# Kernel tuning notes

Measured on AMD Instinct MI355X. Metric: run time of the kernel, lower is better.

The kernel has to match this reference:

```python
import jax, jax.numpy as jnp
import numpy as np

NUM_HEADS = 16


def setup_inputs() -> dict:
    key = jax.random.key(0)
    ks = jax.random.split(key, 6)
    B, S, D = 2, 2048, 1024
    hidden_states = jax.random.normal(ks[0], (B, S, D), dtype=jnp.float32)
    attention_mask = jnp.zeros((B, 1, 1, S), dtype=jnp.float32)  # additive mask
    # Linear weights stored as [in, out] (equivalent to torch weight.T)
    W_qkv = jax.random.normal(ks[1], (D, 3 * D), dtype=jnp.float32) * (1.0 / np.sqrt(D))
    b_qkv = jnp.zeros((3 * D,), dtype=jnp.float32)
    W_proj = jax.random.normal(ks[2], (D, D), dtype=jnp.float32) * (1.0 / np.sqrt(D))
    b_proj = jnp.zeros((D,), dtype=jnp.float32)
    return {
        "hidden_states": hidden_states,
        "attention_mask": attention_mask,
        "W_qkv": W_qkv,
        "b_qkv": b_qkv,
        "W_proj": W_proj,
        "b_proj": b_proj,
    }


def reference(hidden_states, attention_mask, W_qkv, b_qkv, W_proj, b_proj):
    B, S, D = hidden_states.shape
    H = NUM_HEADS
    hd = D // H
    scale = 1.0 / jnp.sqrt(jnp.asarray(hd, hidden_states.dtype))

    qkv = hidden_states @ W_qkv + b_qkv            # [B,S,3D]
    q, k, v = jnp.split(qkv, 3, axis=-1)
    # [B,S,D] -> [B,H,S,hd]
    split_heads = lambda t: t.reshape(B, S, H, hd).transpose(0, 2, 1, 3)
    q, k, v = split_heads(q), split_heads(k), split_heads(v)

    scores = jnp.einsum("bhqd,bhkd->bhqk", q, k) * scale + attention_mask
    attn = jax.nn.softmax(scores, axis=-1)
    ctx = jnp.einsum("bhqk,bhkd->bhqd", attn, v)   # [B,H,S,hd]
    ctx = ctx.transpose(0, 2, 1, 3).reshape(B, S, D)
    return ctx @ W_proj + b_proj
```

## Files before the change

kernel.cpp:

```cpp
#include <hip/hip_runtime.h>
#include <hip/hip_bf16.h>

typedef short short8 __attribute__((ext_vector_type(8)));
typedef float floatx4 __attribute__((ext_vector_type(4)));
typedef int intx4 __attribute__((ext_vector_type(4)));

#define S_LEN 2048
#define DMODEL 1024
#define NH 16
#define HD 64
#define BATCH 2

static __device__ __forceinline__ short f2bf(float x) {
    __hip_bfloat16 h = __float2bfloat16(x);
    return *(short*)&h;
}

static __device__ __forceinline__ unsigned pk2(float lo, float hi) {
    unsigned a = (unsigned)(unsigned short)f2bf(lo);
    unsigned b = (unsigned)(unsigned short)f2bf(hi);
    return a | (b << 16);
}

static __device__ __forceinline__ void async_ld16(const __hip_bfloat16* g, __hip_bfloat16* l) {
    __builtin_amdgcn_global_load_lds(
        (const __attribute__((address_space(1))) unsigned int*)g,
        (__attribute__((address_space(3))) unsigned int*)l, 16, 0, 0);
}

__global__ __launch_bounds__(256) void cvt_kernel(const float* __restrict__ X,
                                                  __hip_bfloat16* __restrict__ Y) {
    int i = (blockIdx.x * 256 + threadIdx.x) * 8;
    floatx4 f0 = *(const floatx4*)&X[i];
    floatx4 f1 = *(const floatx4*)&X[i + 4];
    short8 s;
    s[0] = f2bf(f0[0]); s[1] = f2bf(f0[1]); s[2] = f2bf(f0[2]); s[3] = f2bf(f0[3]);
    s[4] = f2bf(f1[0]); s[5] = f2bf(f1[1]); s[6] = f2bf(f1[2]); s[7] = f2bf(f1[3]);
    *(short8*)&Y[i] = s;
}

__global__ void transpose_kernel(const float* __restrict__ W,
                                 __hip_bfloat16* __restrict__ Wt, int K, int N) {
    __shared__ float tile[32][33];
    int n0 = blockIdx.x * 32, k0 = blockIdx.y * 32;
    int tx = threadIdx.x, ty = threadIdx.y;
#pragma unroll
    for (int i = 0; i < 32; i += 8)
        tile[ty + i][tx] = W[(size_t)(k0 + ty + i) * N + n0 + tx];
    __syncthreads();
#pragma unroll
    for (int i = 0; i < 32; i += 8)
        Wt[(size_t)(n0 + ty + i) * K + k0 + tx] = __float2bfloat16(tile[tx][ty + i]);
}

__global__ __launch_bounds__(256) void gemm128(
    const __hip_bfloat16* __restrict__ A, const __hip_bfloat16* __restrict__ Bt,
    const float* __restrict__ bias, float* __restrict__ Cf,
    __hip_bfloat16* __restrict__ Qp, __hip_bfloat16* __restrict__ Kp,
    __hip_bfloat16* __restrict__ Vt, int M, int N, int K, int mode) {
    __shared__ __align__(16) __hip_bfloat16 As[128 * 32];
    __shared__ __align__(16) __hip_bfloat16 Bs[128 * 32];
    const int m0 = blockIdx.y * 128, n0 = blockIdx.x * 128;
    const int t = threadIdx.x;
    const int wave = t >> 6, lane = t & 63;
    const int quad = lane >> 4, m16 = lane & 15;
    const int wm = (wave >> 1) * 64, wn = (wave & 1) * 64;
    const int srow = lane >> 2, scol = (lane & 3) * 8;

    floatx4 acc[4][4] = {};
    for (int k0 = 0; k0 < K; k0 += 32) {
#pragma unroll
        for (int i = 0; i < 2; i++) {
            const int rbase = wave * 32 + i * 16;
            async_ld16(&A[(size_t)(m0 + rbase + srow) * K + k0 + scol], &As[rbase * 32]);
            async_ld16(&Bt[(size_t)(n0 + rbase + srow) * K + k0 + scol], &Bs[rbase * 32]);
        }
        __syncthreads();
        short8 af[4], bfr[4];
#pragma unroll
        for (int i = 0; i < 4; i++)
            af[i] = *(const short8*)&As[(wm + i * 16 + m16) * 32 + quad * 8];
#pragma unroll
        for (int j = 0; j < 4; j++)
            bfr[j] = *(const short8*)&Bs[(wn + j * 16 + m16) * 32 + quad * 8];
#pragma unroll
        for (int i = 0; i < 4; i++)
#pragma unroll
            for (int j = 0; j < 4; j++)
                acc[i][j] = __builtin_amdgcn_mfma_f32_16x16x32_bf16(af[i], bfr[j], acc[i][j], 0, 0, 0);
        __syncthreads();
    }
#pragma unroll
    for (int i = 0; i < 4; i++)
#pragma unroll
        for (int j = 0; j < 4; j++) {
            int col = n0 + wn + j * 16 + m16;
            float bv = bias[col];
#pragma unroll
            for (int r = 0; r < 4; r++) {
                int row = m0 + wm + i * 16 + quad * 4 + r;
                float v = acc[i][j][r] + bv;
                if (mode == 0) {
                    Cf[(size_t)row * N + col] = v;
                } else {
                    __hip_bfloat16 hv = __float2bfloat16(v);
                    int tt = col >> 10, rem = col & 1023;
                    int h = rem >> 6, d = rem & 63;
                    int b = row >> 11, s = row & 2047;
                    if (tt == 0)      Qp[((size_t)(b * NH + h) * S_LEN + s) * HD + d] = hv;
                    else if (tt == 1) Kp[((size_t)(b * NH + h) * S_LEN + s) * HD + d] = hv;
                    else              Vt[((size_t)(b * NH + h) * HD + d) * S_LEN + s] = hv;
                }
            }
        }
}

__global__ __launch_bounds__(256, 4) void attn_kernel(
    const __hip_bfloat16* __restrict__ Q,
    const __hip_bfloat16* __restrict__ K,
    const __hip_bfloat16* __restrict__ Vt,
    const float* __restrict__ mask,
    __hip_bfloat16* __restrict__ ctx) {
    __shared__ __align__(16) __hip_bfloat16 Ks[2][64 * 64];
    __shared__ __align__(16) __hip_bfloat16 Vs[2][64 * 64];
    const int bh = blockIdx.x;
    const int b = bh >> 4, h = bh & 15;
    const int t = threadIdx.x, wave = t >> 6, lane = t & 63;
    const int quad = lane >> 4, m16 = lane & 15;
    const int qbase = blockIdx.y * 64 + wave * 16;
    const __hip_bfloat16* Qh = Q + (size_t)bh * S_LEN * HD;
    const __hip_bfloat16* Kh = K + (size_t)bh * S_LEN * HD;
    const __hip_bfloat16* Vh = Vt + (size_t)bh * HD * S_LEN;
    const float* mb = mask + (size_t)b * S_LEN;
    const float LOG2E = 1.44269504f;
    const float scale2 = 0.125f * LOG2E;
    const float M_FIX2 = 20.0f * LOG2E;

    const int r8 = lane >> 3, c8 = lane & 7;
    const int kg0 = (wave * 16 + r8) * HD + ((c8 ^ r8) * 8);
    const int kg1 = (wave * 16 + 8 + r8) * HD + ((c8 ^ r8) * 8);
    const int vg0 = (wave * 16 + r8) * S_LEN + ((c8 ^ r8) * 8);
    const int vg1 = (wave * 16 + 8 + r8) * S_LEN + ((c8 ^ r8) * 8);

    short8 aq0 = *(const short8*)&Qh[(size_t)(qbase + m16) * HD + quad * 8];
    short8 aq1 = *(const short8*)&Qh[(size_t)(qbase + m16) * HD + 32 + quad * 8];

    const short ONEB = (short)0x3F80;
    const short8 ones = {ONEB, ONEB, ONEB, ONEB, ONEB, ONEB, ONEB, ONEB};

    {
        __hip_bfloat16* kd = &Ks[0][wave * 16 * 64];
        async_ld16(&Kh[kg0], kd);
        async_ld16(&Kh[kg1], kd + 512);
        __hip_bfloat16* vd = &Vs[0][wave * 16 * 64];
        async_ld16(&Vh[vg0], vd);
        async_ld16(&Vh[vg1], vd + 512);
    }
    __syncthreads();

    floatx4 o[4] = {};
    floatx4 lacc = {};
    const int swk = m16 & 7;
    const int e = quad & 1;
    const int cA = ((quad & 1) << 2) | (quad >> 1);
    const int cB = cA | 2;
    const int vsA = (cA ^ swk) * 8;
    const int vsB = (cB ^ swk) * 8;

    for (int it = 0; it < S_LEN / 64; it++) {
        const int k0 = it * 64;
        const int cur = it & 1;
        if (it < S_LEN / 64 - 1) {
            __hip_bfloat16* kd = &Ks[cur ^ 1][wave * 16 * 64];
            async_ld16(&Kh[(k0 + 64) * HD + kg0], kd);
            async_ld16(&Kh[(k0 + 64) * HD + kg1], kd + 512);
            __hip_bfloat16* vd = &Vs[cur ^ 1][wave * 16 * 64];
            async_ld16(&Vh[(k0 + 64) + vg0], vd);
            async_ld16(&Vh[(k0 + 64) + vg1], vd + 512);
        }

        const __hip_bfloat16* Kc = Ks[cur];
        floatx4 sc[4] = {};
        __builtin_amdgcn_s_setprio(1);
#pragma unroll
        for (int kt = 0; kt < 4; kt++) {
            const int row = kt * 16 + m16;
            short8 ak0 = *(const short8*)&Kc[row * 64 + ((quad ^ swk) * 8)];
            short8 ak1 = *(const short8*)&Kc[row * 64 + (((quad + 4) ^ swk) * 8)];
            sc[kt] = __builtin_amdgcn_mfma_f32_16x16x32_bf16(ak0, aq0, sc[kt], 0, 0, 0);
            sc[kt] = __builtin_amdgcn_mfma_f32_16x16x32_bf16(ak1, aq1, sc[kt], 0, 0, 0);
        }
        __builtin_amdgcn_s_setprio(0);

        unsigned dk[4][2];
#pragma unroll
        for (int kt = 0; kt < 4; kt++) {
            floatx4 mv = *(const floatx4*)&mb[k0 + kt * 16 + quad * 4];
            float p0 = __builtin_amdgcn_exp2f(
                __builtin_fmaf(sc[kt][0], scale2, __builtin_fmaf(mv[0], LOG2E, -M_FIX2)));
            float p1 = __builtin_amdgcn_exp2f(
                __builtin_fmaf(sc[kt][1], scale2, __builtin_fmaf(mv[1], LOG2E, -M_FIX2)));
            float p2 = __builtin_amdgcn_exp2f(
                __builtin_fmaf(sc[kt][2], scale2, __builtin_fmaf(mv[2], LOG2E, -M_FIX2)));
            float p3 = __builtin_amdgcn_exp2f(
                __builtin_fmaf(sc[kt][3], scale2, __builtin_fmaf(mv[3], LOG2E, -M_FIX2)));
            dk[kt][0] = pk2(p0, p1);
            dk[kt][1] = pk2(p2, p3);
        }

        unsigned t0 = e ? dk[0][0] : dk[2][0];
        unsigned t1 = e ? dk[0][1] : dk[2][1];
        unsigned t2 = e ? dk[1][0] : dk[3][0];
        unsigned t3 = e ? dk[1][1] : dk[3][1];
        unsigned r0 = (unsigned)__builtin_amdgcn_ds_swizzle((int)t0, 0x401F);
        unsigned r1 = (unsigned)__builtin_amdgcn_ds_swizzle((int)t1, 0x401F);
        unsigned r2 = (unsigned)__builtin_amdgcn_ds_swizzle((int)t2, 0x401F);
        unsigned r3 = (unsigned)__builtin_amdgcn_ds_swizzle((int)t3, 0x401F);
        intx4 wa, wb;
        wa[0] = (int)(e ? r0 : dk[0][0]);
        wa[1] = (int)(e ? r1 : dk[0][1]);
        wa[2] = (int)(e ? dk[2][0] : r0);
        wa[3] = (int)(e ? dk[2][1] : r1);
        wb[0] = (int)(e ? r2 : dk[1][0]);
        wb[1] = (int)(e ? r3 : dk[1][1]);
        wb[2] = (int)(e ? dk[3][0] : r2);
        wb[3] = (int)(e ? dk[3][1] : r3);
        short8 apA = *(short8*)&wa;
        short8 apB = *(short8*)&wb;

        const __hip_bfloat16* Vc = Vs[cur];
        __builtin_amdgcn_s_setprio(1);
        lacc = __builtin_amdgcn_mfma_f32_16x16x32_bf16(apA, ones, lacc, 0, 0, 0);
        lacc = __builtin_amdgcn_mfma_f32_16x16x32_bf16(apB, ones, lacc, 0, 0, 0);
#pragma unroll
        for (int tt = 0; tt < 4; tt++) {
            const int d = tt * 16 + m16;
            short8 bvA = *(const short8*)&Vc[d * 64 + vsA];
            short8 bvB = *(const short8*)&Vc[d * 64 + vsB];
            o[tt] = __builtin_amdgcn_mfma_f32_16x16x32_bf16(apA, bvA, o[tt], 0, 0, 0);
            o[tt] = __builtin_amdgcn_mfma_f32_16x16x32_bf16(apB, bvB, o[tt], 0, 0, 0);
        }
        __builtin_amdgcn_s_setprio(0);
        __syncthreads();
    }

    float li[4];
#pragma unroll
    for (int r = 0; r < 4; r++) li[r] = 1.0f / lacc[r];
#pragma unroll
    for (int tt = 0; tt < 4; tt++)
#pragma unroll
        for (int r = 0; r < 4; r++) {
            int srow = qbase + quad * 4 + r;
            int d = tt * 16 + m16;
            float v = o[tt][r] * li[r];
            ctx[((size_t)b * S_LEN + srow) * DMODEL + h * HD + d] = __float2bfloat16(v);
        }
}

extern "C" void kernel_launch(void* const* d_in, const int* in_sizes, int n_in,
                              void* d_out, int out_size, void* d_ws, size_t ws_size,
                              hipStream_t stream) {
    (void)in_sizes; (void)n_in; (void)out_size; (void)ws_size;
    const float* hidden = (const float*)d_in[0];
    const float* mask   = (const float*)d_in[1];
    const float* Wqkv   = (const float*)d_in[2];
    const float* bqkv   = (const float*)d_in[3];
    const float* Wproj  = (const float*)d_in[4];
    const float* bproj  = (const float*)d_in[5];
    float* out = (float*)d_out;

    __hip_bfloat16* ws = (__hip_bfloat16*)d_ws;
    const size_t Q4 = 4u * 1024 * 1024;
    __hip_bfloat16* Qp      = ws;
    __hip_bfloat16* Kp      = ws + 1 * Q4;
    __hip_bfloat16* Vt      = ws + 2 * Q4;
    __hip_bfloat16* hid_bf  = ws + 3 * Q4;
    __hip_bfloat16* ctx     = ws + 3 * Q4;
    __hip_bfloat16* Wqkv_t  = ws + 4 * Q4;
    __hip_bfloat16* Wproj_t = ws + 4 * Q4;

    cvt_kernel<<<dim3(4 * 1024 * 1024 / 2048), 256, 0, stream>>>(hidden, hid_bf);
    transpose_kernel<<<dim3(3072 / 32, 1024 / 32), dim3(32, 8), 0, stream>>>(Wqkv, Wqkv_t, 1024, 3072);

    gemm128<<<dim3(3072 / 128, 4096 / 128), 256, 0, stream>>>(
        hid_bf, Wqkv_t, bqkv, nullptr, Qp, Kp, Vt, BATCH * S_LEN, 3 * DMODEL, DMODEL, 1);

    transpose_kernel<<<dim3(1024 / 32, 1024 / 32), dim3(32, 8), 0, stream>>>(Wproj, Wproj_t, 1024, 1024);

    attn_kernel<<<dim3(BATCH * NH, S_LEN / 64), 256, 0, stream>>>(Qp, Kp, Vt, mask, ctx);

    gemm128<<<dim3(1024 / 128, 4096 / 128), 256, 0, stream>>>(
        ctx, Wproj_t, bproj, out, nullptr, nullptr, nullptr, BATCH * S_LEN, DMODEL, DMODEL, 0);
}
```

Baseline: 219.4 us.

## Split attention KV range across two wave teams and merge partials via LDS

The attention block grows from 256 to 512 threads: two teams of four waves each process half of the key sequence for the same 64 queries, using 32-key tiles with their own double-buffered LDS regions. At the end, team 1 writes its partial output and row sums to shared memory and team 0 adds them, normalizes, and writes ctx. The aim is more waves per CU and more latency hiding in the attention stage. The cost is smaller tiles with more barriers per key, an extra LDS exchange and barrier, and tighter register limits from launch_bounds(512,8).

```diff
diff --git a/kernel.cpp b/kernel.cpp
--- a/kernel.cpp
+++ b/kernel.cpp
@@ -115,19 +115,20 @@
         }
 }
 
-__global__ __launch_bounds__(256, 4) void attn_kernel(
+__global__ __launch_bounds__(512, 8) void attn_kernel(
     const __hip_bfloat16* __restrict__ Q,
     const __hip_bfloat16* __restrict__ K,
     const __hip_bfloat16* __restrict__ Vt,
     const float* __restrict__ mask,
     __hip_bfloat16* __restrict__ ctx) {
-    __shared__ __align__(16) __hip_bfloat16 Ks[2][64 * 64];
-    __shared__ __align__(16) __hip_bfloat16 Vs[2][64 * 64];
+    __shared__ __align__(16) __hip_bfloat16 smem[16384];
     const int bh = blockIdx.x;
     const int b = bh >> 4, h = bh & 15;
     const int t = threadIdx.x, wave = t >> 6, lane = t & 63;
+    const int team = wave >> 2, tw = wave & 3;
     const int quad = lane >> 4, m16 = lane & 15;
-    const int qbase = blockIdx.y * 64 + wave * 16;
+    const int qbase = blockIdx.y * 64 + tw * 16;
+    const int ko = team * (S_LEN / 2);
     const __hip_bfloat16* Qh = Q + (size_t)bh * S_LEN * HD;
     const __hip_bfloat16* Kh = K + (size_t)bh * S_LEN * HD;
     const __hip_bfloat16* Vh = Vt + (size_t)bh * HD * S_LEN;
@@ -136,11 +137,18 @@
     const float scale2 = 0.125f * LOG2E;
     const float M_FIX2 = 20.0f * LOG2E;
 
-    const int r8 = lane >> 3, c8 = lane & 7;
-    const int kg0 = (wave * 16 + r8) * HD + ((c8 ^ r8) * 8);
-    const int kg1 = (wave * 16 + 8 + r8) * HD + ((c8 ^ r8) * 8);
-    const int vg0 = (wave * 16 + r8) * S_LEN + ((c8 ^ r8) * 8);
-    const int vg1 = (wave * 16 + 8 + r8) * S_LEN + ((c8 ^ r8) * 8);
+    __hip_bfloat16* Ksb = smem + team * 8192;
+    __hip_bfloat16* Vsb = smem + team * 8192 + 4096;
+
+    const int kr = lane >> 3, kc = lane & 7;
+    const int kgoff = (tw * 8 + kr) * HD + ((kc ^ kr) * 8);
+    const int vr = lane >> 2, vc = lane & 3;
+    const int vd = tw * 16 + vr;
+    const int vgoff = vd * S_LEN + (((vc ^ ((vd >> 1) & 3))) * 8);
+    __hip_bfloat16* kdst0 = Ksb + tw * 512;
+    __hip_bfloat16* kdst1 = Ksb + 2048 + tw * 512;
+    __hip_bfloat16* vdst0 = Vsb + tw * 512;
+    __hip_bfloat16* vdst1 = Vsb + 2048 + tw * 512;
 
     short8 aq0 = *(const short8*)&Qh[(size_t)(qbase + m16) * HD + quad * 8];
     short8 aq1 = *(const short8*)&Qh[(size_t)(qbase + m16) * HD + 32 + quad * 8];
@@ -148,42 +156,31 @@
     const short ONEB = (short)0x3F80;
     const short8 ones = {ONEB, ONEB, ONEB, ONEB, ONEB, ONEB, ONEB, ONEB};
 
-    {
-        __hip_bfloat16* kd = &Ks[0][wave * 16 * 64];
-        async_ld16(&Kh[kg0], kd);
-        async_ld16(&Kh[kg1], kd + 512);
-        __hip_bfloat16* vd = &Vs[0][wave * 16 * 64];
-        async_ld16(&Vh[vg0], vd);
-        async_ld16(&Vh[vg1], vd + 512);
-    }
+    async_ld16(&Kh[(size_t)ko * HD + kgoff], kdst0);
+    async_ld16(&Vh[(size_t)ko + vgoff], vdst0);
     __syncthreads();
 
     floatx4 o[4] = {};
     floatx4 lacc = {};
     const int swk = m16 & 7;
     const int e = quad & 1;
-    const int cA = ((quad & 1) << 2) | (quad >> 1);
-    const int cB = cA | 2;
-    const int vsA = (cA ^ swk) * 8;
-    const int vsB = (cB ^ swk) * 8;
-
-    for (int it = 0; it < S_LEN / 64; it++) {
-        const int k0 = it * 64;
+    const int C = ((quad & 1) << 1) | (quad >> 1);
+    const int vsl = (C ^ ((m16 >> 1) & 3)) * 8;
+
+    const int NIT = (S_LEN / 2) / 32;
+    for (int it = 0; it < NIT; it++) {
+        const int k0 = it * 32;
         const int cur = it & 1;
-        if (it < S_LEN / 64 - 1) {
-            __hip_bfloat16* kd = &Ks[cur ^ 1][wave * 16 * 64];
-            async_ld16(&Kh[(k0 + 64) * HD + kg0], kd);
-            async_ld16(&Kh[(k0 + 64) * HD + kg1], kd + 512);
-            __hip_bfloat16* vd = &Vs[cur ^ 1][wave * 16 * 64];
-            async_ld16(&Vh[(k0 + 64) + vg0], vd);
-            async_ld16(&Vh[(k0 + 64) + vg1], vd + 512);
-        }
-
-        const __hip_bfloat16* Kc = Ks[cur];
-        floatx4 sc[4] = {};
+        if (it < NIT - 1) {
+            async_ld16(&Kh[(size_t)(ko + k0 + 32) * HD + kgoff], cur ? kdst0 : kdst1);
+            async_ld16(&Vh[(size_t)(ko + k0 + 32) + vgoff], cur ? vdst0 : vdst1);
+        }
+
+        const __hip_bfloat16* Kc = Ksb + cur * 2048;
+        floatx4 sc[2] = {};
         __builtin_amdgcn_s_setprio(1);
 #pragma unroll
-        for (int kt = 0; kt < 4; kt++) {
+        for (int kt = 0; kt < 2; kt++) {
             const int row = kt * 16 + m16;
             short8 ak0 = *(const short8*)&Kc[row * 64 + ((quad ^ swk) * 8)];
             short8 ak1 = *(const short8*)&Kc[row * 64 + (((quad + 4) ^ swk) * 8)];
@@ -192,10 +189,10 @@
         }
         __builtin_amdgcn_s_setprio(0);
 
-        unsigned dk[4][2];
-#pragma unroll
-        for (int kt = 0; kt < 4; kt++) {
-            floatx4 mv = *(const floatx4*)&mb[k0 + kt * 16 + quad * 4];
+        unsigned dk[2][2];
+#pragma unroll
+        for (int kt = 0; kt < 2; kt++) {
+            floatx4 mv = *(const floatx4*)&mb[ko + k0 + kt * 16 + quad * 4];
             float p0 = __builtin_amdgcn_exp2f(
                 __builtin_fmaf(sc[kt][0], scale2, __builtin_fmaf(mv[0], LOG2E, -M_FIX2)));
             float p1 = __builtin_amdgcn_exp2f(
@@ -208,54 +205,55 @@
             dk[kt][1] = pk2(p2, p3);
         }
 
-        unsigned t0 = e ? dk[0][0] : dk[2][0];
-        unsigned t1 = e ? dk[0][1] : dk[2][1];
-        unsigned t2 = e ? dk[1][0] : dk[3][0];
-        unsigned t3 = e ? dk[1][1] : dk[3][1];
-        unsigned r0 = (unsigned)__builtin_amdgcn_ds_swizzle((int)t0, 0x401F);
-        unsigned r1 = (unsigned)__builtin_amdgcn_ds_swizzle((int)t1, 0x401F);
-        unsigned r2 = (unsigned)__builtin_amdgcn_ds_swizzle((int)t2, 0x401F);
-        unsigned r3 = (unsigned)__builtin_amdgcn_ds_swizzle((int)t3, 0x401F);
-        intx4 wa, wb;
+        unsigned s0 = e ? dk[0][0] : dk[1][0];
+        unsigned s1 = e ? dk[0][1] : dk[1][1];
+        unsigned r0 = (unsigned)__builtin_amdgcn_ds_swizzle((int)s0, 0x401F);
+        unsigned r1 = (unsigned)__builtin_amdgcn_ds_swizzle((int)s1, 0x401F);
+        intx4 wa;
         wa[0] = (int)(e ? r0 : dk[0][0]);
         wa[1] = (int)(e ? r1 : dk[0][1]);
-        wa[2] = (int)(e ? dk[2][0] : r0);
-        wa[3] = (int)(e ? dk[2][1] : r1);
-        wb[0] = (int)(e ? r2 : dk[1][0]);
-        wb[1] = (int)(e ? r3 : dk[1][1]);
-        wb[2] = (int)(e ? dk[3][0] : r2);
-        wb[3] = (int)(e ? dk[3][1] : r3);
-        short8 apA = *(short8*)&wa;
-        short8 apB = *(short8*)&wb;
-
-        const __hip_bfloat16* Vc = Vs[cur];
+        wa[2] = (int)(e ? dk[1][0] : r0);
+        wa[3] = (int)(e ? dk[1][1] : r1);
+        short8 ap = *(short8*)&wa;
+
+        const __hip_bfloat16* Vc = Vsb + cur * 2048;
         __builtin_amdgcn_s_setprio(1);
-        lacc = __builtin_amdgcn_mfma_f32_16x16x32_bf16(apA, ones, lacc, 0, 0, 0);
-        lacc = __builtin_amdgcn_mfma_f32_16x16x32_bf16(apB, ones, lacc, 0, 0, 0);
+        lacc = __builtin_amdgcn_mfma_f32_16x16x32_bf16(ap, ones, lacc, 0, 0, 0);
 #pragma unroll
         for (int tt = 0; tt < 4; tt++) {
             const int d = tt * 16 + m16;
-            short8 bvA = *(const short8*)&Vc[d * 64 + vsA];
-            short8 bvB = *(const short8*)&Vc[d * 64 + vsB];
-            o[tt] = __builtin_amdgcn_mfma_f32_16x16x32_bf16(apA, bvA, o[tt], 0, 0, 0);
-            o[tt] = __builtin_amdgcn_mfma_f32_16x16x32_bf16(apB, bvB, o[tt], 0, 0, 0);
+            short8 bv = *(const short8*)&Vc[d * 32 + vsl];
+            o[tt] = __builtin_amdgcn_mfma_f32_16x16x32_bf16(ap, bv, o[tt], 0, 0, 0);
         }
         __builtin_amdgcn_s_setprio(0);
         __syncthreads();
     }
 
-    float li[4];
-#pragma unroll
-    for (int r = 0; r < 4; r++) li[r] = 1.0f / lacc[r];
-#pragma unroll
-    for (int tt = 0; tt < 4; tt++)
-#pragma unroll
-        for (int r = 0; r < 4; r++) {
-            int srow = qbase + quad * 4 + r;
-            int d = tt * 16 + m16;
-            float v = o[tt][r] * li[r];
-            ctx[((size_t)b * S_LEN + srow) * DMODEL + h * HD + d] = __float2bfloat16(v);
-        }
+    float* xch = (float*)smem;
+    const int xi = (tw * 64 + lane) * 21;
+    if (team == 1) {
+#pragma unroll
+        for (int tt = 0; tt < 4; tt++)
+#pragma unroll
+            for (int r = 0; r < 4; r++) xch[xi + tt * 4 + r] = o[tt][r];
+#pragma unroll
+        for (int r = 0; r < 4; r++) xch[xi + 16 + r] = lacc[r];
+    }
+    __syncthreads();
+    if (team == 0) {
+        float li[4];
+#pragma unroll
+        for (int r = 0; r < 4; r++) li[r] = 1.0f / (lacc[r] + xch[xi + 16 + r]);
+#pragma unroll
+        for (int tt = 0; tt < 4; tt++)
+#pragma unroll
+            for (int r = 0; r < 4; r++) {
+                int srow = qbase + quad * 4 + r;
+                int d = tt * 16 + m16;
+                float v = (o[tt][r] + xch[xi + tt * 4 + r]) * li[r];
+                ctx[((size_t)b * S_LEN + srow) * DMODEL + h * HD + d] = __float2bfloat16(v);
+            }
+    }
 }
 
 extern "C" void kernel_launch(void* const* d_in, const int* in_sizes, int n_in,
@@ -288,7 +286,7 @@
 
     transpose_kernel<<<dim3(1024 / 32, 1024 / 32), dim3(32, 8), 0, stream>>>(Wproj, Wproj_t, 1024, 1024);
 
-    attn_kernel<<<dim3(BATCH * NH, S_LEN / 64), 256, 0, stream>>>(Qp, Kp, Vt, mask, ctx);
+    attn_kernel<<<dim3(BATCH * NH, S_LEN / 64), 512, 0, stream>>>(Qp, Kp, Vt, mask, ctx);
 
     gemm128<<<dim3(1024 / 128, 4096 / 128), 256, 0, stream>>>(
         ctx, Wproj_t, bproj, out, nullptr, nullptr, nullptr, BATCH * S_LEN, DMODEL, DMODEL, 0);
```

After: 218.7 us. About the same (-0.3%).
